# Kernel optimization log

Measured on AMD Instinct MI355X. Metric: run time of the kernel, lower is better.

Reference implementation:

```python
import jax, jax.numpy as jnp
import numpy as np

NUM_QRYS = 300
NUM_CLASSES = 80
NUM_PAIRS = 4_000_000
NMS_CANDIDATES = 1000
NMS_THR = 0.65
MAX_SEGS = 100
REFINED_WEIGHT = 2.0
FH = FW = 256  # final mask grid resolution


def setup_inputs() -> dict:
    key = jax.random.key(0)
    k1, k2, k3, k4, k5, k6, k7 = jax.random.split(key, 7)
    cls_logits = jax.random.normal(k1, (NUM_QRYS, NUM_CLASSES + 1), jnp.float32)
    # valid xyxy boxes in normalized [0,1] coords
    b = jax.random.uniform(k2, (NUM_QRYS, 4), jnp.float32)
    x1 = b[:, 0] * 0.7
    y1 = b[:, 1] * 0.7
    x2 = x1 + 0.05 + b[:, 2] * 0.25
    y2 = y1 + 0.05 + b[:, 3] * 0.25
    pred_boxes = jnp.stack([x1, y1, x2, y2], axis=1)
    seg_logits = jax.random.normal(k3, (NUM_PAIRS,), jnp.float32)
    key_xy = jax.random.uniform(k4, (NUM_PAIRS, 2), jnp.float32)
    qry_ids = jax.random.randint(k5, (NUM_PAIRS,), 0, NUM_QRYS, jnp.int32)
    refined_mask = jax.random.randint(k6, (NUM_PAIRS,), 0, 2, jnp.int32).astype(bool)
    map_ids = jax.random.randint(k7, (NUM_PAIRS,), 0, 4, jnp.int32)
    return {"cls_logits": cls_logits, "pred_boxes": pred_boxes, "seg_logits": seg_logits,
            "key_xy": key_xy, "qry_ids": qry_ids, "refined_mask": refined_mask, "map_ids": map_ids}


def _box_iou(boxes):  # boxes: [C,4] xyxy -> [C,C]
    x1 = jnp.maximum(boxes[:, None, 0], boxes[None, :, 0])
    y1 = jnp.maximum(boxes[:, None, 1], boxes[None, :, 1])
    x2 = jnp.minimum(boxes[:, None, 2], boxes[None, :, 2])
    y2 = jnp.minimum(boxes[:, None, 3], boxes[None, :, 3])
    inter = jnp.clip(x2 - x1, 0.0) * jnp.clip(y2 - y1, 0.0)
    area = (boxes[:, 2] - boxes[:, 0]) * (boxes[:, 3] - boxes[:, 1])
    union = area[:, None] + area[None, :] - inter
    return inter / jnp.maximum(union, 1e-9)


def _nms_keep(iou, thr):
    # greedy NMS over score-sorted candidates (rows already in descending score order)
    C = iou.shape[0]
    idx = jnp.arange(C)
    def body(i, keep):
        sup = (iou[i] > thr) & (idx > i) & keep[i]
        return keep & ~sup
    return jax.lax.fori_loop(0, C, body, jnp.ones(C, dtype=bool))


def reference(cls_logits, pred_boxes, seg_logits, key_xy, qry_ids, refined_mask, map_ids):
    num_qrys = cls_logits.shape[0]
    # expand per-query class scores -> flat predictions (batch_size = 1)
    scores = jax.nn.sigmoid(cls_logits[:, :-1]).reshape(-1)          # [Q*C]
    feat_ids = jnp.repeat(jnp.arange(num_qrys), NUM_CLASSES)          # [Q*C]
    labels = jnp.tile(jnp.arange(NUM_CLASSES), num_qrys)              # [Q*C]
    # top-k candidates before NMS
    top_scores, cand = jax.lax.top_k(scores, NMS_CANDIDATES)
    cand_feats = feat_ids[cand]
    cand_labels = labels[cand]
    # class-aware (batched) NMS: offset boxes per label so classes don't suppress each other
    offs = cand_labels.astype(pred_boxes.dtype)[:, None] * 4.0
    cand_boxes = pred_boxes[cand_feats] + offs
    keep = _nms_keep(_box_iou(cand_boxes), NMS_THR)
    kept_scores = jnp.where(keep, top_scores, -jnp.inf)
    sel_scores, sel = jax.lax.top_k(kept_scores, MAX_SEGS)
    sel_scores = jnp.where(jnp.isfinite(sel_scores), sel_scores, 0.0)
    sel_feats = cand_feats[sel]
    # assemble per-query mask logit maps from sparse query-key pairs (scatter-max)
    px = jnp.clip((key_xy[:, 0] * FW).astype(jnp.int32), 0, FW - 1)
    py = jnp.clip((key_xy[:, 1] * FH).astype(jnp.int32), 0, FH - 1)
    w_logits = jnp.where(refined_mask, REFINED_WEIGHT * seg_logits, seg_logits)
    flat = qry_ids * (FH * FW) + py * FW + px                          # [num_pairs]
    qry_maps = jnp.full((num_qrys * FH * FW,), -1e4, cls_logits.dtype).at[flat].max(w_logits)
    qry_maps = qry_maps.reshape(num_qrys, FH, FW)
    mask_probs = jax.nn.sigmoid(qry_maps[sel_feats])                   # [MAX_SEGS, FH, FW]
    # score-weighted soft masks (float output; thresholding at mask_thr yields bool masks)
    return sel_scores[:, None, None] * mask_probs
```

## Files before the change

### kernel.cpp

```cpp
#include <hip/hip_runtime.h>

#define NQ        300
#define NC        80
#define NE        24000
#define CAND      1000
#define KSEL      100
#define NPAIRS    4000000
#define HB        4096
#define FHW       65536
#define NMS_THR_F 0.65f
#define MAPS_INIT 0x39E3BFFFu
#define INIT_VEC4 1638400

typedef unsigned long long ull;

__device__ __forceinline__ unsigned enc_f32(float f) {
    unsigned u = __float_as_uint(f);
    return (u & 0x80000000u) ? ~u : (u | 0x80000000u);
}
__device__ __forceinline__ float dec_f32(unsigned k) {
    unsigned u = (k & 0x80000000u) ? (k ^ 0x80000000u) : ~k;
    return __uint_as_float(u);
}

__global__ __launch_bounds__(1024) void k_front(
    const float* __restrict__ cls,
    const float* __restrict__ pboxes,
    const unsigned* __restrict__ refined_raw,
    uint4* __restrict__ maps4, ull* __restrict__ keys_g,
    float* __restrict__ sel_score_g, int* __restrict__ sel_slot_g,
    int* __restrict__ qry2slot_g, unsigned* __restrict__ mode_flag_g)
{
    if (blockIdx.x > 0) {
        uint4 v; v.x = v.y = v.z = v.w = MAPS_INIT;
        for (int i = (int)(blockIdx.x - 1) * 1024 + (int)threadIdx.x;
             i < INIT_VEC4; i += 256 * 1024)
            maps4[i] = v;
        return;
    }

    __shared__ ull sbuf[4096];
    __shared__ float sbx[CAND], sby[CAND], sbz[CAND], sbw[CAND];
    __shared__ float sscore[CAND];
    __shared__ short sfeat[CAND];
    __shared__ unsigned char slab[CAND];
    __shared__ unsigned char skeep[CAND];
    __shared__ int wlist[16][64];
    __shared__ int q2s[NQ];
    __shared__ float ss[KSEL]; __shared__ int sf[KSEL];
    __shared__ unsigned subhist[64];
    __shared__ unsigned smode;
    __shared__ int sB, sT, sAbove, sCount, sN;

    unsigned* hist = (unsigned*)sbuf;
    int tid = threadIdx.x;
    int lane = tid & 63, wv = tid >> 6;

    for (int b = tid; b < HB; b += 1024) hist[b] = 0u;
    if (tid < 64) subhist[tid] = 0u;
    if (tid == 0) { smode = 0u; sCount = 0; sB = 0; sAbove = 0; }
    __syncthreads();

    #pragma unroll
    for (int k = 0; k < 24; k++) {
        int e = tid + (k << 10);
        if (e < NE) {
            int q = e / NC, c = e - q * NC;
            float x = cls[q * (NC + 1) + c];
            float s = 1.f / (1.f + expf(-x));
            unsigned bits = __float_as_uint(s);
            keys_g[e] = ((ull)bits << 32) | (unsigned)(0xFFFFFFFFu - (unsigned)e);
            atomicAdd(&hist[bits >> 18], 1u);
        }
    }
    if (refined_raw[tid] > 1u) atomicOr(&smode, 1u);
    __syncthreads();

    if (tid < 64) {
        int acc = 0;
        for (int base = HB - 64; base >= 0; base -= 64) {
            unsigned h = hist[base + lane];
            unsigned r = h;
            #pragma unroll
            for (int d = 1; d < 64; d <<= 1) {
                unsigned t2 = __shfl_down(r, d, 64);
                if (lane + d < 64) r += t2;
            }
            ull m = __ballot(acc + (int)r >= CAND);
            if (m) {
                int hi = 63 - __clzll(m);
                int rB = __shfl((int)r, hi, 64);
                int hB = __shfl((int)h, hi, 64);
                if (lane == 0) { sB = base + hi; sAbove = acc + rB - hB; }
                break;
            }
            acc += __shfl((int)r, 0, 64);
        }
    }
    __syncthreads();
    unsigned B = (unsigned)sB;

    #pragma unroll
    for (int k = 0; k < 24; k++) {
        int e = tid + (k << 10);
        if (e < NE) {
            ull key = keys_g[e];
            if ((unsigned)(key >> 50) == B)
                atomicAdd(&subhist[(unsigned)(key >> 44) & 63u], 1u);
        }
    }
    __syncthreads();
    if (tid < 64) {
        unsigned h = subhist[lane];
        unsigned r = h;
        #pragma unroll
        for (int d = 1; d < 64; d <<= 1) {
            unsigned t2 = __shfl_down(r, d, 64);
            if (lane + d < 64) r += t2;
        }
        int above = sAbove;
        ull m = __ballot(above + (int)r >= CAND);
        int hi = 63 - __clzll(m);
        int rT = __shfl((int)r, hi, 64);
        if (lane == 0) { sT = hi; sN = above + rT; }
    }
    __syncthreads();
    unsigned T = (unsigned)sT;

    #pragma unroll
    for (int k = 0; k < 24; k++) {
        int e = tid + (k << 10);
        if (e < NE) {
            ull key = keys_g[e];
            unsigned bkt = (unsigned)(key >> 50);
            unsigned sub = (unsigned)(key >> 44) & 63u;
            if (bkt > B || (bkt == B && sub >= T)) {
                int pos = atomicAdd(&sCount, 1);
                if (pos < 4096) sbuf[pos] = key;
            }
        }
    }
    __syncthreads();
    int n = min(sN, 4096);

    if (n <= 1024) {
        ull r = (tid < n) ? sbuf[tid] : 0ULL;
        for (int k = 2; k <= 1024; k <<= 1) {
            for (int j = k >> 1; j > 0; j >>= 1) {
                ull p;
                if (j >= 64) {
                    sbuf[tid] = r; __syncthreads();
                    p = sbuf[tid ^ j]; __syncthreads();
                } else {
                    p = __shfl_xor(r, j, 64);
                }
                bool d = (tid & k) != 0, lower = (tid & j) == 0;
                r = (d != lower) ? (r > p ? r : p) : (r < p ? r : p);
            }
        }
        sbuf[tid] = r;
        __syncthreads();
    } else {
        int nsort = 2048; while (nsort < n) nsort <<= 1;
        for (int i = n + tid; i < nsort; i += 1024) sbuf[i] = 0ULL;
        __syncthreads();
        for (int k = 2; k <= nsort; k <<= 1)
            for (int j = k >> 1; j > 0; j >>= 1) {
                for (int i = tid; i < nsort; i += 1024) {
                    int ixj = i ^ j;
                    if (ixj > i) {
                        ull a = sbuf[i], b2 = sbuf[ixj];
                        bool up = ((i & k) == 0);
                        if (up ? (a < b2) : (a > b2)) { sbuf[i] = b2; sbuf[ixj] = a; }
                    }
                }
                __syncthreads();
            }
    }

    if (tid < CAND) {
        ull key = sbuf[tid];
        unsigned bits = (unsigned)(key >> 32);
        unsigned e = 0xFFFFFFFFu - (unsigned)(key & 0xFFFFFFFFu);
        int feat = (int)e / NC, lab = (int)e - feat * NC;
        sscore[tid] = __uint_as_float(bits);
        sfeat[tid]  = (short)feat;
        slab[tid]   = (unsigned char)lab;
        float off = 4.f * (float)lab;
        const float4 pb = ((const float4*)pboxes)[feat];
        sbx[tid] = pb.x + off; sby[tid] = pb.y + off;
        sbz[tid] = pb.z + off; sbw[tid] = pb.w + off;
    }
    __syncthreads();

    for (int li = 0; li < 5; li++) {
        int lab = wv + (li << 4);
        int nb = 0;
        for (int c = 0; c < CAND; c += 64) {
            int i = c + lane;
            bool m = (i < CAND) && ((int)slab[i] == lab);
            ull bal = __ballot(m);
            if (m) {
                int r = nb + __popcll(bal & ((1ULL << lane) - 1ULL));
                if (r < 64) wlist[wv][r] = i;
            }
            nb += __popcll(bal);
        }
        int nl = min(nb, 64);
        __syncthreads();

        bool alive = lane < nl;
        float bxv = 0.f, byv = 0.f, bzv = 0.f, bwv = 0.f, ar = 0.f;
        int idx = -1;
        if (alive) {
            idx = wlist[wv][lane];
            bxv = sbx[idx]; byv = sby[idx]; bzv = sbz[idx]; bwv = sbw[idx];
            ar = (bzv - bxv) * (bwv - byv);
        }
        bool keep = alive;
        for (int i = 0; i < nl; i++) {
            float bix = __shfl(bxv, i), biy = __shfl(byv, i);
            float biz = __shfl(bzv, i), biw = __shfl(bwv, i);
            float ai  = __shfl(ar, i);
            int   ki  = __shfl((int)keep, i);
            if (ki && keep && lane > i) {
                float xx1 = fmaxf(bix, bxv), yy1 = fmaxf(biy, byv);
                float xx2 = fminf(biz, bzv), yy2 = fminf(biw, bwv);
                float inter = fmaxf(xx2 - xx1, 0.f) * fmaxf(yy2 - yy1, 0.f);
                float uni = ai + ar - inter;
                if (inter / fmaxf(uni, 1e-9f) > NMS_THR_F) keep = false;
            }
        }
        if (alive) skeep[idx] = keep ? 1 : 0;
    }
    __syncthreads();

    for (int q = tid; q < NQ; q += 1024) q2s[q] = -1;
    __syncthreads();
    if (tid < 64) {
        int base = 0;
        for (int c = 0; c < CAND; c += 64) {
            int i = c + lane;
            bool k2 = (i < CAND) && skeep[i];
            ull bal = __ballot(k2);
            int pos = base + __popcll(bal & ((1ULL << lane) - 1ULL));
            if (k2 && pos < KSEL) { ss[pos] = sscore[i]; sf[pos] = (int)sfeat[i]; }
            base += __popcll(bal);
        }
        int nsel = min(base, KSEL);
        int s1 = lane, s2 = lane + 64;
        int fp1 = s1, fp2 = s2;
        if (s1 < nsel) { int f = sf[s1]; for (int k2 = 0; k2 < s1; k2++) if (sf[k2] == f) { fp1 = k2; break; } }
        if (s2 < nsel) { int f = sf[s2]; for (int k2 = 0; k2 < s2; k2++) if (sf[k2] == f) { fp2 = k2; break; } }
        bool fo1 = (s1 < nsel) && (fp1 == s1);
        bool fo2 = (s2 < nsel) && (fp2 == s2);
        ull b1 = __ballot(fo1);
        ull b2 = __ballot(fo2);
        int c1 = __popcll(b1);
        int slot1 = -1, slot2 = -1;
        if (s1 < nsel) slot1 = __popcll(b1 & ((1ULL << fp1) - 1ULL));
        if (s2 < nsel) slot2 = (fp2 < 64) ? __popcll(b1 & ((1ULL << fp2) - 1ULL))
                                          : c1 + __popcll(b2 & ((1ULL << (fp2 - 64)) - 1ULL));
        sel_slot_g[s1] = slot1;
        sel_score_g[s1] = (s1 < nsel) ? ss[s1] : 0.f;
        if (s2 < KSEL) {
            sel_slot_g[s2] = slot2;
            sel_score_g[s2] = (s2 < nsel) ? ss[s2] : 0.f;
        }
        if (fo1) q2s[sf[s1]] = slot1;
        if (fo2) q2s[sf[s2]] = slot2;
        if (lane == 0) *mode_flag_g = smode;
    }
    __syncthreads();
    for (int q = tid; q < NQ; q += 1024) qry2slot_g[q] = q2s[q];
}

__global__ __launch_bounds__(256) void k_scatter(
    const float* __restrict__ seg, const float2* __restrict__ xy,
    const int* __restrict__ qry, const unsigned* __restrict__ refined_raw,
    const int* __restrict__ qry2slot, const unsigned* __restrict__ mode_flag,
    unsigned* __restrict__ maps)
{
    int t = blockIdx.x * 256 + threadIdx.x;
    if ((t << 2) >= NPAIRS) return;

    int4 q4     = ((const int4*)qry)[t];
    float4 sg   = ((const float4*)seg)[t];
    float4 xy01 = ((const float4*)xy)[2 * t];
    float4 xy23 = ((const float4*)xy)[2 * t + 1];
    unsigned r0, r1, r2, r3;
    if (*mode_flag) {
        unsigned rb = refined_raw[t];
        r0 = rb & 255u; r1 = (rb >> 8) & 255u; r2 = (rb >> 16) & 255u; r3 = rb >> 24;
    } else {
        uint4 rr = ((const uint4*)refined_raw)[t];
        r0 = rr.x; r1 = rr.y; r2 = rr.z; r3 = rr.w;
    }
    int s0 = qry2slot[q4.x], s1 = qry2slot[q4.y];
    int s2 = qry2slot[q4.z], s3 = qry2slot[q4.w];

    #define DO_PAIR(S, PX, PY, W, R)                                              \
        if (S >= 0) {                                                             \
            int px = min(max((int)((PX) * 256.f), 0), 255);                       \
            int py = min(max((int)((PY) * 256.f), 0), 255);                       \
            float w = (R) ? 2.f * (W) : (W);                                      \
            atomicMax(&maps[S * FHW + py * 256 + px], enc_f32(w));                \
        }
    DO_PAIR(s0, xy01.x, xy01.y, sg.x, r0)
    DO_PAIR(s1, xy01.z, xy01.w, sg.y, r1)
    DO_PAIR(s2, xy23.x, xy23.y, sg.z, r2)
    DO_PAIR(s3, xy23.z, xy23.w, sg.w, r3)
    #undef DO_PAIR
}

__global__ __launch_bounds__(256) void k_output(
    const uint4* __restrict__ maps4,
    const float* __restrict__ sel_score, const int* __restrict__ sel_slot,
    float4* __restrict__ out4)
{
    int i = blockIdx.x * 256 + threadIdx.x;
    int s = i >> 14;
    float sc = sel_score[s];
    int slot = sel_slot[s];
    float4 v = {0.f, 0.f, 0.f, 0.f};
    if (slot >= 0) {
        uint4 m = maps4[slot * (FHW / 4) + (i & 16383)];
        v.x = sc / (1.f + expf(-dec_f32(m.x)));
        v.y = sc / (1.f + expf(-dec_f32(m.y)));
        v.z = sc / (1.f + expf(-dec_f32(m.z)));
        v.w = sc / (1.f + expf(-dec_f32(m.w)));
    }
    out4[i] = v;
}

extern "C" void kernel_launch(void* const* d_in, const int* in_sizes, int n_in,
                              void* d_out, int out_size, void* d_ws, size_t ws_size,
                              hipStream_t stream) {
    const float*    cls     = (const float*)d_in[0];
    const float*    pboxes  = (const float*)d_in[1];
    const float*    seg     = (const float*)d_in[2];
    const float2*   xy      = (const float2*)d_in[3];
    const int*      qry     = (const int*)d_in[4];
    const unsigned* refined = (const unsigned*)d_in[5];
    float* out = (float*)d_out;

    char* ws = (char*)d_ws;
    unsigned*  maps      = (unsigned*)ws;
    float*     sel_score = (float*)   (ws + 26214400);
    int*       sel_slot  = (int*)     (ws + 26214800);
    int*       qry2slot  = (int*)     (ws + 26215200);
    unsigned*  mode_flag = (unsigned*)(ws + 26216400);
    ull*       keys      = (ull*)d_out;

    k_front  <<<257, 1024, 0, stream>>>(cls, pboxes, refined, (uint4*)maps, keys,
                                        sel_score, sel_slot, qry2slot, mode_flag);
    k_scatter<<<3907, 256, 0, stream>>>(seg, xy, qry, refined, qry2slot, mode_flag, maps);
    k_output <<<6400, 256, 0, stream>>>((const uint4*)maps, sel_score, sel_slot,
                                        (float4*)out);
}
```

Before: 253.4 us.

## Split monolithic front kernel into multi-block init, histogram, boundary, sort and NMS stages

Breaks the single-block front kernel into separate launches. Map init and the sigmoid/key/histogram work now run across many blocks, and a finer 65536-bin global histogram locates the top-1000 boundary in one pass, with no sub-histogram refinement. The serial single-block part now covers only the 2048-wide bitonic sort and the NMS. The cost is more kernel launches and global-memory handoffs between the stages. The sort buffer is capped at 2048, which assumes boundary-bucket ties stay small.

```diff
diff --git a/kernel.cpp b/kernel.cpp
--- a/kernel.cpp
+++ b/kernel.cpp
@@ -6,11 +6,10 @@
 #define CAND      1000
 #define KSEL      100
 #define NPAIRS    4000000
-#define HB        4096
+#define HBN       65536
 #define FHW       65536
 #define NMS_THR_F 0.65f
 #define MAPS_INIT 0x39E3BFFFu
-#define INIT_VEC4 1638400
 
 typedef unsigned long long ull;
 
@@ -23,125 +22,93 @@
     return __uint_as_float(u);
 }
 
-__global__ __launch_bounds__(1024) void k_front(
-    const float* __restrict__ cls,
-    const float* __restrict__ pboxes,
-    const unsigned* __restrict__ refined_raw,
-    uint4* __restrict__ maps4, ull* __restrict__ keys_g,
-    float* __restrict__ sel_score_g, int* __restrict__ sel_slot_g,
-    int* __restrict__ qry2slot_g, unsigned* __restrict__ mode_flag_g)
-{
-    if (blockIdx.x > 0) {
+__global__ void k_init(uint4* __restrict__ maps4, unsigned* __restrict__ hist,
+                       unsigned* __restrict__ mode_flag) {
+    int b = blockIdx.x, tid = threadIdx.x;
+    if (b < 6400) {
         uint4 v; v.x = v.y = v.z = v.w = MAPS_INIT;
-        for (int i = (int)(blockIdx.x - 1) * 1024 + (int)threadIdx.x;
-             i < INIT_VEC4; i += 256 * 1024)
-            maps4[i] = v;
-        return;
-    }
-
-    __shared__ ull sbuf[4096];
-    __shared__ float sbx[CAND], sby[CAND], sbz[CAND], sbw[CAND];
-    __shared__ float sscore[CAND];
-    __shared__ short sfeat[CAND];
-    __shared__ unsigned char slab[CAND];
-    __shared__ unsigned char skeep[CAND];
-    __shared__ int wlist[16][64];
-    __shared__ int q2s[NQ];
-    __shared__ float ss[KSEL]; __shared__ int sf[KSEL];
-    __shared__ unsigned subhist[64];
-    __shared__ unsigned smode;
-    __shared__ int sB, sT, sAbove, sCount, sN;
-
-    unsigned* hist = (unsigned*)sbuf;
+        maps4[b * 256 + tid] = v;
+    } else {
+        int j = (b - 6400) * 256 + tid;
+        if (j < HBN) hist[j] = 0u;
+        if (j == HBN) *mode_flag = 0u;
+    }
+}
+
+__global__ __launch_bounds__(256) void k_sigkeys(
+    const float* __restrict__ cls, const unsigned* __restrict__ refined_raw,
+    ull* __restrict__ keys_g, unsigned* __restrict__ hist,
+    unsigned* __restrict__ mode_flag)
+{
     int tid = threadIdx.x;
-    int lane = tid & 63, wv = tid >> 6;
-
-    for (int b = tid; b < HB; b += 1024) hist[b] = 0u;
-    if (tid < 64) subhist[tid] = 0u;
-    if (tid == 0) { smode = 0u; sCount = 0; sB = 0; sAbove = 0; }
-    __syncthreads();
-
-    #pragma unroll
-    for (int k = 0; k < 24; k++) {
-        int e = tid + (k << 10);
-        if (e < NE) {
-            int q = e / NC, c = e - q * NC;
-            float x = cls[q * (NC + 1) + c];
-            float s = 1.f / (1.f + expf(-x));
-            unsigned bits = __float_as_uint(s);
-            keys_g[e] = ((ull)bits << 32) | (unsigned)(0xFFFFFFFFu - (unsigned)e);
-            atomicAdd(&hist[bits >> 18], 1u);
-        }
-    }
-    if (refined_raw[tid] > 1u) atomicOr(&smode, 1u);
-    __syncthreads();
-
-    if (tid < 64) {
-        int acc = 0;
-        for (int base = HB - 64; base >= 0; base -= 64) {
-            unsigned h = hist[base + lane];
-            unsigned r = h;
-            #pragma unroll
-            for (int d = 1; d < 64; d <<= 1) {
-                unsigned t2 = __shfl_down(r, d, 64);
-                if (lane + d < 64) r += t2;
-            }
-            ull m = __ballot(acc + (int)r >= CAND);
-            if (m) {
-                int hi = 63 - __clzll(m);
-                int rB = __shfl((int)r, hi, 64);
-                int hB = __shfl((int)h, hi, 64);
-                if (lane == 0) { sB = base + hi; sAbove = acc + rB - hB; }
-                break;
-            }
-            acc += __shfl((int)r, 0, 64);
-        }
-    }
-    __syncthreads();
-    unsigned B = (unsigned)sB;
+    int e = blockIdx.x * 256 + tid;
+    if (e < NE) {
+        int q = e / NC, c = e - q * NC;
+        float x = cls[q * (NC + 1) + c];
+        float s = 1.f / (1.f + expf(-x));
+        unsigned bits = __float_as_uint(s);
+        keys_g[e] = ((ull)bits << 32) | (unsigned)(0xFFFFFFFFu - (unsigned)e);
+        atomicAdd(&hist[min(bits >> 14, (unsigned)(HBN - 1))], 1u);
+    }
+    if (blockIdx.x == 0) {
+        unsigned bad = 0;
+        #pragma unroll
+        for (int j = 0; j < 4; j++) bad |= (refined_raw[tid + 256 * j] > 1u) ? 1u : 0u;
+        if (bad) atomicOr(mode_flag, 1u);
+    }
+}
+
+__global__ __launch_bounds__(64) void k_boundary(
+    const unsigned* __restrict__ hist, int* __restrict__ bn)
+{
+    int lane = threadIdx.x;
+    int acc = 0;
+    for (int base = HBN - 64; base >= 0; base -= 64) {
+        unsigned h = hist[base + lane];
+        unsigned r = h;
+        #pragma unroll
+        for (int d = 1; d < 64; d <<= 1) {
+            unsigned t2 = __shfl_down(r, d, 64);
+            if (lane + d < 64) r += t2;
+        }
+        ull m = __ballot(acc + (int)r >= CAND);
+        if (m) {
+            int hi = 63 - __clzll(m);
+            int rB = __shfl((int)r, hi, 64);
+            if (lane == 0) { bn[0] = base + hi; bn[1] = acc + rB; }
+            return;
+        }
+        acc += __shfl((int)r, 0, 64);
+    }
+    if (lane == 0) { bn[0] = 0; bn[1] = NE; }
+}
+
+__global__ __launch_bounds__(1024) void k_sortsel(
+    const ull* __restrict__ keys_g, const float* __restrict__ pboxes,
+    const int* __restrict__ bn,
+    float4* __restrict__ cboxes, float* __restrict__ cscore,
+    int* __restrict__ cfeat, int* __restrict__ clabel)
+{
+    __shared__ ull sbuf[2048];
+    __shared__ int sCount;
+    int tid = threadIdx.x;
+    if (tid == 0) sCount = 0;
+    __syncthreads();
+    unsigned B = (unsigned)bn[0];
 
     #pragma unroll
     for (int k = 0; k < 24; k++) {
         int e = tid + (k << 10);
         if (e < NE) {
             ull key = keys_g[e];
-            if ((unsigned)(key >> 50) == B)
-                atomicAdd(&subhist[(unsigned)(key >> 44) & 63u], 1u);
-        }
-    }
-    __syncthreads();
-    if (tid < 64) {
-        unsigned h = subhist[lane];
-        unsigned r = h;
-        #pragma unroll
-        for (int d = 1; d < 64; d <<= 1) {
-            unsigned t2 = __shfl_down(r, d, 64);
-            if (lane + d < 64) r += t2;
-        }
-        int above = sAbove;
-        ull m = __ballot(above + (int)r >= CAND);
-        int hi = 63 - __clzll(m);
-        int rT = __shfl((int)r, hi, 64);
-        if (lane == 0) { sT = hi; sN = above + rT; }
-    }
-    __syncthreads();
-    unsigned T = (unsigned)sT;
-
-    #pragma unroll
-    for (int k = 0; k < 24; k++) {
-        int e = tid + (k << 10);
-        if (e < NE) {
-            ull key = keys_g[e];
-            unsigned bkt = (unsigned)(key >> 50);
-            unsigned sub = (unsigned)(key >> 44) & 63u;
-            if (bkt > B || (bkt == B && sub >= T)) {
+            if ((unsigned)(key >> 46) >= B) {
                 int pos = atomicAdd(&sCount, 1);
-                if (pos < 4096) sbuf[pos] = key;
-            }
-        }
-    }
-    __syncthreads();
-    int n = min(sN, 4096);
+                if (pos < 2048) sbuf[pos] = key;
+            }
+        }
+    }
+    __syncthreads();
+    int n = min(sCount, 2048);
 
     if (n <= 1024) {
         ull r = (tid < n) ? sbuf[tid] : 0ULL;
@@ -161,12 +128,11 @@
         sbuf[tid] = r;
         __syncthreads();
     } else {
-        int nsort = 2048; while (nsort < n) nsort <<= 1;
-        for (int i = n + tid; i < nsort; i += 1024) sbuf[i] = 0ULL;
+        for (int i = n + tid; i < 2048; i += 1024) sbuf[i] = 0ULL;
         __syncthreads();
-        for (int k = 2; k <= nsort; k <<= 1)
+        for (int k = 2; k <= 2048; k <<= 1)
             for (int j = k >> 1; j > 0; j >>= 1) {
-                for (int i = tid; i < nsort; i += 1024) {
+                for (int i = tid; i < 2048; i += 1024) {
                     int ixj = i ^ j;
                     if (ixj > i) {
                         ull a = sbuf[i], b2 = sbuf[ixj];
@@ -183,22 +149,35 @@
         unsigned bits = (unsigned)(key >> 32);
         unsigned e = 0xFFFFFFFFu - (unsigned)(key & 0xFFFFFFFFu);
         int feat = (int)e / NC, lab = (int)e - feat * NC;
-        sscore[tid] = __uint_as_float(bits);
-        sfeat[tid]  = (short)feat;
-        slab[tid]   = (unsigned char)lab;
+        cscore[tid] = __uint_as_float(bits);
+        cfeat[tid]  = feat;
+        clabel[tid] = lab;
         float off = 4.f * (float)lab;
-        const float4 pb = ((const float4*)pboxes)[feat];
-        sbx[tid] = pb.x + off; sby[tid] = pb.y + off;
-        sbz[tid] = pb.z + off; sbw[tid] = pb.w + off;
-    }
-    __syncthreads();
+        float4 pb = ((const float4*)pboxes)[feat];
+        float4 b;
+        b.x = pb.x + off; b.y = pb.y + off; b.z = pb.z + off; b.w = pb.w + off;
+        cboxes[tid] = b;
+    }
+}
+
+__global__ __launch_bounds__(1024) void k_nms_pick(
+    const float4* __restrict__ cboxes, const float* __restrict__ cscore,
+    const int* __restrict__ cfeat, const int* __restrict__ clabel,
+    float* __restrict__ sel_score_g, int* __restrict__ sel_slot_g,
+    int* __restrict__ qry2slot_g)
+{
+    __shared__ unsigned char skeep[CAND];
+    __shared__ int wlist[16][64];
+    __shared__ int q2s[NQ];
+    __shared__ float ss[KSEL]; __shared__ int sf[KSEL];
+    int tid = threadIdx.x, lane = tid & 63, wv = tid >> 6;
 
     for (int li = 0; li < 5; li++) {
         int lab = wv + (li << 4);
         int nb = 0;
         for (int c = 0; c < CAND; c += 64) {
             int i = c + lane;
-            bool m = (i < CAND) && ((int)slab[i] == lab);
+            bool m = (i < CAND) && (clabel[i] == lab);
             ull bal = __ballot(m);
             if (m) {
                 int r = nb + __popcll(bal & ((1ULL << lane) - 1ULL));
@@ -214,7 +193,8 @@
         int idx = -1;
         if (alive) {
             idx = wlist[wv][lane];
-            bxv = sbx[idx]; byv = sby[idx]; bzv = sbz[idx]; bwv = sbw[idx];
+            float4 cb = cboxes[idx];
+            bxv = cb.x; byv = cb.y; bzv = cb.z; bwv = cb.w;
             ar = (bzv - bxv) * (bwv - byv);
         }
         bool keep = alive;
@@ -244,7 +224,7 @@
             bool k2 = (i < CAND) && skeep[i];
             ull bal = __ballot(k2);
             int pos = base + __popcll(bal & ((1ULL << lane) - 1ULL));
-            if (k2 && pos < KSEL) { ss[pos] = sscore[i]; sf[pos] = (int)sfeat[i]; }
+            if (k2 && pos < KSEL) { ss[pos] = cscore[i]; sf[pos] = cfeat[i]; }
             base += __popcll(bal);
         }
         int nsel = min(base, KSEL);
@@ -269,7 +249,6 @@
         }
         if (fo1) q2s[sf[s1]] = slot1;
         if (fo2) q2s[sf[s2]] = slot2;
-        if (lane == 0) *mode_flag_g = smode;
     }
     __syncthreads();
     for (int q = tid; q < NQ; q += 1024) qry2slot_g[q] = q2s[q];
@@ -344,17 +323,29 @@
     const unsigned* refined = (const unsigned*)d_in[5];
     float* out = (float*)d_out;
 
+    char* ob = (char*)d_out;
+    ull*      keys   = (ull*)ob;
+    unsigned* hist   = (unsigned*)(ob + 196608);
+    float4*   cboxes = (float4*)(ob + 458752);
+    float*    cscore = (float*)(ob + 474752);
+    int*      cfeat  = (int*)(ob + 478752);
+    int*      clabel = (int*)(ob + 482752);
+    int*      bn     = (int*)(ob + 486752);
+
     char* ws = (char*)d_ws;
-    unsigned*  maps      = (unsigned*)ws;
-    float*     sel_score = (float*)   (ws + 26214400);
-    int*       sel_slot  = (int*)     (ws + 26214800);
-    int*       qry2slot  = (int*)     (ws + 26215200);
-    unsigned*  mode_flag = (unsigned*)(ws + 26216400);
-    ull*       keys      = (ull*)d_out;
-
-    k_front  <<<257, 1024, 0, stream>>>(cls, pboxes, refined, (uint4*)maps, keys,
-                                        sel_score, sel_slot, qry2slot, mode_flag);
-    k_scatter<<<3907, 256, 0, stream>>>(seg, xy, qry, refined, qry2slot, mode_flag, maps);
-    k_output <<<6400, 256, 0, stream>>>((const uint4*)maps, sel_score, sel_slot,
-                                        (float4*)out);
-}
+    unsigned* maps      = (unsigned*)ws;
+    float*    sel_score = (float*)   (ws + 26214400);
+    int*      sel_slot  = (int*)     (ws + 26214800);
+    int*      qry2slot  = (int*)     (ws + 26215200);
+    unsigned* mode_flag = (unsigned*)(ws + 26216400);
+
+    k_init    <<<6657, 256, 0, stream>>>((uint4*)maps, hist, mode_flag);
+    k_sigkeys <<<94, 256, 0, stream>>>(cls, refined, keys, hist, mode_flag);
+    k_boundary<<<1, 64, 0, stream>>>(hist, bn);
+    k_sortsel <<<1, 1024, 0, stream>>>(keys, pboxes, bn, cboxes, cscore, cfeat, clabel);
+    k_nms_pick<<<1, 1024, 0, stream>>>(cboxes, cscore, cfeat, clabel,
+                                       sel_score, sel_slot, qry2slot);
+    k_scatter <<<3907, 256, 0, stream>>>(seg, xy, qry, refined, qry2slot, mode_flag, maps);
+    k_output  <<<6400, 256, 0, stream>>>((const uint4*)maps, sel_score, sel_slot,
+                                         (float4*)out);
+}
```

Result: no change. 254.4 us (+0.4%).

## Fuse all stages into one cooperative persistent kernel with grid syncs

Applied to the files above, without the earlier changes.

Merges the front (top-k, NMS), scatter and output kernels into a single cooperative kernel of 256 blocks of 1024 threads, separated by grid.sync barriers. The candidate histogram is built grid-wide with a finer 65536-bucket global histogram, replacing the two-level shared-memory selection. This removes launch gaps between kernels, but the scatter and output stages now run at the lower occupancy of a persistent grid, and several grid syncs are added. The single-block sort and NMS phase still serialises while the other blocks wait at the barrier.

```diff
diff --git a/kernel.cpp b/kernel.cpp
--- a/kernel.cpp
+++ b/kernel.cpp
@@ -1,4 +1,7 @@
 #include <hip/hip_runtime.h>
+#include <hip/hip_cooperative_groups.h>
+
+namespace cg = cooperative_groups;
 
 #define NQ        300
 #define NC        80
@@ -6,11 +9,13 @@
 #define CAND      1000
 #define KSEL      100
 #define NPAIRS    4000000
-#define HB        4096
+#define HBN       65536
 #define FHW       65536
 #define NMS_THR_F 0.65f
 #define MAPS_INIT 0x39E3BFFFu
-#define INIT_VEC4 1638400
+#define GBLK      256
+#define GTH       262144
+#define MAPS_V4   1638400
 
 typedef unsigned long long ull;
 
@@ -23,314 +28,283 @@
     return __uint_as_float(u);
 }
 
-__global__ __launch_bounds__(1024) void k_front(
+__global__ __launch_bounds__(1024) void k_mega(
     const float* __restrict__ cls,
     const float* __restrict__ pboxes,
-    const unsigned* __restrict__ refined_raw,
-    uint4* __restrict__ maps4, ull* __restrict__ keys_g,
-    float* __restrict__ sel_score_g, int* __restrict__ sel_slot_g,
-    int* __restrict__ qry2slot_g, unsigned* __restrict__ mode_flag_g)
+    const float* __restrict__ seg, const float2* __restrict__ xy,
+    const int* __restrict__ qry, const unsigned* __restrict__ refined,
+    unsigned* __restrict__ maps, ull* __restrict__ keys,
+    unsigned* __restrict__ hist, ull* __restrict__ cand,
+    int* __restrict__ cand_count,
+    float* __restrict__ sel_score, int* __restrict__ sel_slot,
+    int* __restrict__ qry2slot, unsigned* __restrict__ mode_flag,
+    float* __restrict__ out)
 {
-    if (blockIdx.x > 0) {
-        uint4 v; v.x = v.y = v.z = v.w = MAPS_INIT;
-        for (int i = (int)(blockIdx.x - 1) * 1024 + (int)threadIdx.x;
-             i < INIT_VEC4; i += 256 * 1024)
-            maps4[i] = v;
-        return;
-    }
-
-    __shared__ ull sbuf[4096];
+    cg::grid_group grid = cg::this_grid();
+    const int tid = threadIdx.x, bid = blockIdx.x;
+    const int flat = bid * 1024 + tid;
+    const int lane = tid & 63;
+
+    __shared__ ull sbuf[2048];
     __shared__ float sbx[CAND], sby[CAND], sbz[CAND], sbw[CAND];
     __shared__ float sscore[CAND];
     __shared__ short sfeat[CAND];
-    __shared__ unsigned char slab[CAND];
-    __shared__ unsigned char skeep[CAND];
+    __shared__ unsigned char slab[CAND], skeep[CAND];
     __shared__ int wlist[16][64];
     __shared__ int q2s[NQ];
     __shared__ float ss[KSEL]; __shared__ int sf[KSEL];
-    __shared__ unsigned subhist[64];
-    __shared__ unsigned smode;
-    __shared__ int sB, sT, sAbove, sCount, sN;
-
-    unsigned* hist = (unsigned*)sbuf;
-    int tid = threadIdx.x;
-    int lane = tid & 63, wv = tid >> 6;
-
-    for (int b = tid; b < HB; b += 1024) hist[b] = 0u;
-    if (tid < 64) subhist[tid] = 0u;
-    if (tid == 0) { smode = 0u; sCount = 0; sB = 0; sAbove = 0; }
-    __syncthreads();
-
-    #pragma unroll
-    for (int k = 0; k < 24; k++) {
-        int e = tid + (k << 10);
-        if (e < NE) {
-            int q = e / NC, c = e - q * NC;
-            float x = cls[q * (NC + 1) + c];
-            float s = 1.f / (1.f + expf(-x));
-            unsigned bits = __float_as_uint(s);
-            keys_g[e] = ((ull)bits << 32) | (unsigned)(0xFFFFFFFFu - (unsigned)e);
-            atomicAdd(&hist[bits >> 18], 1u);
-        }
-    }
-    if (refined_raw[tid] > 1u) atomicOr(&smode, 1u);
-    __syncthreads();
-
-    if (tid < 64) {
-        int acc = 0;
-        for (int base = HB - 64; base >= 0; base -= 64) {
-            unsigned h = hist[base + lane];
-            unsigned r = h;
-            #pragma unroll
-            for (int d = 1; d < 64; d <<= 1) {
-                unsigned t2 = __shfl_down(r, d, 64);
-                if (lane + d < 64) r += t2;
-            }
-            ull m = __ballot(acc + (int)r >= CAND);
-            if (m) {
-                int hi = 63 - __clzll(m);
-                int rB = __shfl((int)r, hi, 64);
-                int hB = __shfl((int)h, hi, 64);
-                if (lane == 0) { sB = base + hi; sAbove = acc + rB - hB; }
-                break;
-            }
-            acc += __shfl((int)r, 0, 64);
-        }
-    }
-    __syncthreads();
-    unsigned B = (unsigned)sB;
-
-    #pragma unroll
-    for (int k = 0; k < 24; k++) {
-        int e = tid + (k << 10);
-        if (e < NE) {
-            ull key = keys_g[e];
-            if ((unsigned)(key >> 50) == B)
-                atomicAdd(&subhist[(unsigned)(key >> 44) & 63u], 1u);
-        }
-    }
-    __syncthreads();
-    if (tid < 64) {
-        unsigned h = subhist[lane];
-        unsigned r = h;
-        #pragma unroll
-        for (int d = 1; d < 64; d <<= 1) {
-            unsigned t2 = __shfl_down(r, d, 64);
-            if (lane + d < 64) r += t2;
-        }
-        int above = sAbove;
-        ull m = __ballot(above + (int)r >= CAND);
-        int hi = 63 - __clzll(m);
-        int rT = __shfl((int)r, hi, 64);
-        if (lane == 0) { sT = hi; sN = above + rT; }
-    }
-    __syncthreads();
-    unsigned T = (unsigned)sT;
-
-    #pragma unroll
-    for (int k = 0; k < 24; k++) {
-        int e = tid + (k << 10);
-        if (e < NE) {
-            ull key = keys_g[e];
-            unsigned bkt = (unsigned)(key >> 50);
-            unsigned sub = (unsigned)(key >> 44) & 63u;
-            if (bkt > B || (bkt == B && sub >= T)) {
-                int pos = atomicAdd(&sCount, 1);
-                if (pos < 4096) sbuf[pos] = key;
-            }
-        }
-    }
-    __syncthreads();
-    int n = min(sN, 4096);
-
-    if (n <= 1024) {
-        ull r = (tid < n) ? sbuf[tid] : 0ULL;
-        for (int k = 2; k <= 1024; k <<= 1) {
-            for (int j = k >> 1; j > 0; j >>= 1) {
-                ull p;
-                if (j >= 64) {
-                    sbuf[tid] = r; __syncthreads();
-                    p = sbuf[tid ^ j]; __syncthreads();
-                } else {
-                    p = __shfl_xor(r, j, 64);
-                }
-                bool d = (tid & k) != 0, lower = (tid & j) == 0;
-                r = (d != lower) ? (r > p ? r : p) : (r < p ? r : p);
-            }
-        }
-        sbuf[tid] = r;
-        __syncthreads();
-    } else {
-        int nsort = 2048; while (nsort < n) nsort <<= 1;
-        for (int i = n + tid; i < nsort; i += 1024) sbuf[i] = 0ULL;
-        __syncthreads();
-        for (int k = 2; k <= nsort; k <<= 1)
-            for (int j = k >> 1; j > 0; j >>= 1) {
-                for (int i = tid; i < nsort; i += 1024) {
-                    int ixj = i ^ j;
-                    if (ixj > i) {
-                        ull a = sbuf[i], b2 = sbuf[ixj];
-                        bool up = ((i & k) == 0);
-                        if (up ? (a < b2) : (a > b2)) { sbuf[i] = b2; sbuf[ixj] = a; }
+    __shared__ int sB;
+    __shared__ unsigned smode_l;
+
+    {
+        uint4 v; v.x = v.y = v.z = v.w = MAPS_INIT;
+        uint4* maps4 = (uint4*)maps;
+        for (int i = flat; i < MAPS_V4; i += GTH) maps4[i] = v;
+        if (flat < HBN) hist[flat] = 0u;
+        if (flat == 0) *cand_count = 0;
+    }
+    grid.sync();
+
+    if (flat < NE) {
+        int q = flat / NC, c = flat - q * NC;
+        float x = cls[q * (NC + 1) + c];
+        float s = 1.f / (1.f + expf(-x));
+        unsigned bits = __float_as_uint(s);
+        keys[flat] = ((ull)bits << 32) | (unsigned)(0xFFFFFFFFu - (unsigned)flat);
+        atomicAdd(&hist[min(bits >> 14, (unsigned)(HBN - 1))], 1u);
+    }
+    if (bid == 24) {
+        if (tid == 0) smode_l = 0u;
+        __syncthreads();
+        if (refined[tid] > 1u) atomicOr(&smode_l, 1u);
+        __syncthreads();
+        if (tid == 0) *mode_flag = smode_l;
+    }
+    grid.sync();
+
+    if (bid < 24) {
+        if (tid < 64) {
+            int acc = 0;
+            for (int b2 = HBN - 64; b2 >= 0; b2 -= 64) {
+                unsigned h = hist[b2 + lane];
+                unsigned r = h;
+                #pragma unroll
+                for (int d = 1; d < 64; d <<= 1) {
+                    unsigned t2 = __shfl_down(r, d, 64);
+                    if (lane + d < 64) r += t2;
+                }
+                ull m = __ballot(acc + (int)r >= CAND);
+                if (m) {
+                    if (lane == 0) sB = b2 + (63 - __clzll(m));
+                    break;
+                }
+                acc += __shfl((int)r, 0, 64);
+            }
+        }
+        __syncthreads();
+        unsigned B = (unsigned)sB;
+        bool q = false; ull key = 0ULL;
+        if (flat < NE) {
+            key = keys[flat];
+            q = ((unsigned)(key >> 46) >= B);
+        }
+        ull bal = __ballot(q);
+        int rank = __popcll(bal & ((1ULL << lane) - 1ULL));
+        int base = 0;
+        if (lane == 0 && bal) base = atomicAdd(cand_count, (int)__popcll(bal));
+        base = __shfl(base, 0, 64);
+        if (q) cand[base + rank] = key;
+    }
+    grid.sync();
+
+    if (bid == 0) {
+        int n = min(*cand_count, 2048);
+        for (int i = tid; i < 2048; i += 1024) sbuf[i] = (i < n) ? cand[i] : 0ULL;
+        __syncthreads();
+
+        if (n <= 1024) {
+            ull r = sbuf[tid];
+            for (int k = 2; k <= 1024; k <<= 1) {
+                for (int j = k >> 1; j > 0; j >>= 1) {
+                    ull p;
+                    if (j >= 64) {
+                        sbuf[tid] = r; __syncthreads();
+                        p = sbuf[tid ^ j]; __syncthreads();
+                    } else {
+                        p = __shfl_xor(r, j, 64);
                     }
-                }
-                __syncthreads();
-            }
-    }
-
-    if (tid < CAND) {
-        ull key = sbuf[tid];
-        unsigned bits = (unsigned)(key >> 32);
-        unsigned e = 0xFFFFFFFFu - (unsigned)(key & 0xFFFFFFFFu);
-        int feat = (int)e / NC, lab = (int)e - feat * NC;
-        sscore[tid] = __uint_as_float(bits);
-        sfeat[tid]  = (short)feat;
-        slab[tid]   = (unsigned char)lab;
-        float off = 4.f * (float)lab;
-        const float4 pb = ((const float4*)pboxes)[feat];
-        sbx[tid] = pb.x + off; sby[tid] = pb.y + off;
-        sbz[tid] = pb.z + off; sbw[tid] = pb.w + off;
-    }
-    __syncthreads();
-
-    for (int li = 0; li < 5; li++) {
-        int lab = wv + (li << 4);
-        int nb = 0;
-        for (int c = 0; c < CAND; c += 64) {
-            int i = c + lane;
-            bool m = (i < CAND) && ((int)slab[i] == lab);
-            ull bal = __ballot(m);
-            if (m) {
-                int r = nb + __popcll(bal & ((1ULL << lane) - 1ULL));
-                if (r < 64) wlist[wv][r] = i;
-            }
-            nb += __popcll(bal);
-        }
-        int nl = min(nb, 64);
-        __syncthreads();
-
-        bool alive = lane < nl;
-        float bxv = 0.f, byv = 0.f, bzv = 0.f, bwv = 0.f, ar = 0.f;
-        int idx = -1;
-        if (alive) {
-            idx = wlist[wv][lane];
-            bxv = sbx[idx]; byv = sby[idx]; bzv = sbz[idx]; bwv = sbw[idx];
-            ar = (bzv - bxv) * (bwv - byv);
-        }
-        bool keep = alive;
-        for (int i = 0; i < nl; i++) {
-            float bix = __shfl(bxv, i), biy = __shfl(byv, i);
-            float biz = __shfl(bzv, i), biw = __shfl(bwv, i);
-            float ai  = __shfl(ar, i);
-            int   ki  = __shfl((int)keep, i);
-            if (ki && keep && lane > i) {
-                float xx1 = fmaxf(bix, bxv), yy1 = fmaxf(biy, byv);
-                float xx2 = fminf(biz, bzv), yy2 = fminf(biw, bwv);
-                float inter = fmaxf(xx2 - xx1, 0.f) * fmaxf(yy2 - yy1, 0.f);
-                float uni = ai + ar - inter;
-                if (inter / fmaxf(uni, 1e-9f) > NMS_THR_F) keep = false;
-            }
-        }
-        if (alive) skeep[idx] = keep ? 1 : 0;
-    }
-    __syncthreads();
-
-    for (int q = tid; q < NQ; q += 1024) q2s[q] = -1;
-    __syncthreads();
-    if (tid < 64) {
-        int base = 0;
-        for (int c = 0; c < CAND; c += 64) {
-            int i = c + lane;
-            bool k2 = (i < CAND) && skeep[i];
-            ull bal = __ballot(k2);
-            int pos = base + __popcll(bal & ((1ULL << lane) - 1ULL));
-            if (k2 && pos < KSEL) { ss[pos] = sscore[i]; sf[pos] = (int)sfeat[i]; }
-            base += __popcll(bal);
-        }
-        int nsel = min(base, KSEL);
-        int s1 = lane, s2 = lane + 64;
-        int fp1 = s1, fp2 = s2;
-        if (s1 < nsel) { int f = sf[s1]; for (int k2 = 0; k2 < s1; k2++) if (sf[k2] == f) { fp1 = k2; break; } }
-        if (s2 < nsel) { int f = sf[s2]; for (int k2 = 0; k2 < s2; k2++) if (sf[k2] == f) { fp2 = k2; break; } }
-        bool fo1 = (s1 < nsel) && (fp1 == s1);
-        bool fo2 = (s2 < nsel) && (fp2 == s2);
-        ull b1 = __ballot(fo1);
-        ull b2 = __ballot(fo2);
-        int c1 = __popcll(b1);
-        int slot1 = -1, slot2 = -1;
-        if (s1 < nsel) slot1 = __popcll(b1 & ((1ULL << fp1) - 1ULL));
-        if (s2 < nsel) slot2 = (fp2 < 64) ? __popcll(b1 & ((1ULL << fp2) - 1ULL))
-                                          : c1 + __popcll(b2 & ((1ULL << (fp2 - 64)) - 1ULL));
-        sel_slot_g[s1] = slot1;
-        sel_score_g[s1] = (s1 < nsel) ? ss[s1] : 0.f;
-        if (s2 < KSEL) {
-            sel_slot_g[s2] = slot2;
-            sel_score_g[s2] = (s2 < nsel) ? ss[s2] : 0.f;
-        }
-        if (fo1) q2s[sf[s1]] = slot1;
-        if (fo2) q2s[sf[s2]] = slot2;
-        if (lane == 0) *mode_flag_g = smode;
-    }
-    __syncthreads();
-    for (int q = tid; q < NQ; q += 1024) qry2slot_g[q] = q2s[q];
-}
-
-__global__ __launch_bounds__(256) void k_scatter(
-    const float* __restrict__ seg, const float2* __restrict__ xy,
-    const int* __restrict__ qry, const unsigned* __restrict__ refined_raw,
-    const int* __restrict__ qry2slot, const unsigned* __restrict__ mode_flag,
-    unsigned* __restrict__ maps)
-{
-    int t = blockIdx.x * 256 + threadIdx.x;
-    if ((t << 2) >= NPAIRS) return;
-
-    int4 q4     = ((const int4*)qry)[t];
-    float4 sg   = ((const float4*)seg)[t];
-    float4 xy01 = ((const float4*)xy)[2 * t];
-    float4 xy23 = ((const float4*)xy)[2 * t + 1];
-    unsigned r0, r1, r2, r3;
-    if (*mode_flag) {
-        unsigned rb = refined_raw[t];
-        r0 = rb & 255u; r1 = (rb >> 8) & 255u; r2 = (rb >> 16) & 255u; r3 = rb >> 24;
-    } else {
-        uint4 rr = ((const uint4*)refined_raw)[t];
-        r0 = rr.x; r1 = rr.y; r2 = rr.z; r3 = rr.w;
-    }
-    int s0 = qry2slot[q4.x], s1 = qry2slot[q4.y];
-    int s2 = qry2slot[q4.z], s3 = qry2slot[q4.w];
-
-    #define DO_PAIR(S, PX, PY, W, R)                                              \
-        if (S >= 0) {                                                             \
-            int px = min(max((int)((PX) * 256.f), 0), 255);                       \
-            int py = min(max((int)((PY) * 256.f), 0), 255);                       \
-            float w = (R) ? 2.f * (W) : (W);                                      \
-            atomicMax(&maps[S * FHW + py * 256 + px], enc_f32(w));                \
-        }
-    DO_PAIR(s0, xy01.x, xy01.y, sg.x, r0)
-    DO_PAIR(s1, xy01.z, xy01.w, sg.y, r1)
-    DO_PAIR(s2, xy23.x, xy23.y, sg.z, r2)
-    DO_PAIR(s3, xy23.z, xy23.w, sg.w, r3)
-    #undef DO_PAIR
-}
-
-__global__ __launch_bounds__(256) void k_output(
-    const uint4* __restrict__ maps4,
-    const float* __restrict__ sel_score, const int* __restrict__ sel_slot,
-    float4* __restrict__ out4)
-{
-    int i = blockIdx.x * 256 + threadIdx.x;
-    int s = i >> 14;
-    float sc = sel_score[s];
-    int slot = sel_slot[s];
-    float4 v = {0.f, 0.f, 0.f, 0.f};
-    if (slot >= 0) {
-        uint4 m = maps4[slot * (FHW / 4) + (i & 16383)];
-        v.x = sc / (1.f + expf(-dec_f32(m.x)));
-        v.y = sc / (1.f + expf(-dec_f32(m.y)));
-        v.z = sc / (1.f + expf(-dec_f32(m.z)));
-        v.w = sc / (1.f + expf(-dec_f32(m.w)));
-    }
-    out4[i] = v;
+                    bool d = (tid & k) != 0, lower = (tid & j) == 0;
+                    r = (d != lower) ? (r > p ? r : p) : (r < p ? r : p);
+                }
+            }
+            sbuf[tid] = r;
+            __syncthreads();
+        } else {
+            for (int k = 2; k <= 2048; k <<= 1)
+                for (int j = k >> 1; j > 0; j >>= 1) {
+                    for (int i = tid; i < 2048; i += 1024) {
+                        int ixj = i ^ j;
+                        if (ixj > i) {
+                            ull a = sbuf[i], b2 = sbuf[ixj];
+                            bool up = ((i & k) == 0);
+                            if (up ? (a < b2) : (a > b2)) { sbuf[i] = b2; sbuf[ixj] = a; }
+                        }
+                    }
+                    __syncthreads();
+                }
+        }
+
+        if (tid < CAND) {
+            ull key = sbuf[tid];
+            unsigned bits = (unsigned)(key >> 32);
+            unsigned e = 0xFFFFFFFFu - (unsigned)(key & 0xFFFFFFFFu);
+            int feat = (int)e / NC, lab = (int)e - feat * NC;
+            sscore[tid] = __uint_as_float(bits);
+            sfeat[tid]  = (short)feat;
+            slab[tid]   = (unsigned char)lab;
+            skeep[tid]  = 0;
+            float off = 4.f * (float)lab;
+            float4 pb = ((const float4*)pboxes)[feat];
+            sbx[tid] = pb.x + off; sby[tid] = pb.y + off;
+            sbz[tid] = pb.z + off; sbw[tid] = pb.w + off;
+        }
+        __syncthreads();
+
+        int wv = tid >> 6;
+        for (int li = 0; li < 5; li++) {
+            int lab = wv + (li << 4);
+            int nb = 0;
+            for (int c = 0; c < CAND; c += 64) {
+                int i = c + lane;
+                bool m = (i < CAND) && ((int)slab[i] == lab);
+                ull bal = __ballot(m);
+                if (m) {
+                    int r = nb + __popcll(bal & ((1ULL << lane) - 1ULL));
+                    if (r < 64) wlist[wv][r] = i;
+                }
+                nb += __popcll(bal);
+            }
+            int nl = min(nb, 64);
+            __syncthreads();
+
+            bool alive = lane < nl;
+            float bxv = 0.f, byv = 0.f, bzv = 0.f, bwv = 0.f, ar = 0.f;
+            int idx = -1;
+            if (alive) {
+                idx = wlist[wv][lane];
+                bxv = sbx[idx]; byv = sby[idx]; bzv = sbz[idx]; bwv = sbw[idx];
+                ar = (bzv - bxv) * (bwv - byv);
+            }
+            bool keep = alive;
+            for (int i = 0; i < nl; i++) {
+                float bix = __shfl(bxv, i), biy = __shfl(byv, i);
+                float biz = __shfl(bzv, i), biw = __shfl(bwv, i);
+                float ai  = __shfl(ar, i);
+                int   ki  = __shfl((int)keep, i);
+                if (ki && keep && lane > i) {
+                    float xx1 = fmaxf(bix, bxv), yy1 = fmaxf(biy, byv);
+                    float xx2 = fminf(biz, bzv), yy2 = fminf(biw, bwv);
+                    float inter = fmaxf(xx2 - xx1, 0.f) * fmaxf(yy2 - yy1, 0.f);
+                    float uni = ai + ar - inter;
+                    if (inter / fmaxf(uni, 1e-9f) > NMS_THR_F) keep = false;
+                }
+            }
+            if (alive) skeep[idx] = keep ? 1 : 0;
+        }
+        __syncthreads();
+
+        for (int q = tid; q < NQ; q += 1024) q2s[q] = -1;
+        __syncthreads();
+        if (tid < 64) {
+            int base = 0;
+            for (int c = 0; c < CAND; c += 64) {
+                int i = c + lane;
+                bool k2 = (i < CAND) && skeep[i];
+                ull bal = __ballot(k2);
+                int pos = base + __popcll(bal & ((1ULL << lane) - 1ULL));
+                if (k2 && pos < KSEL) { ss[pos] = sscore[i]; sf[pos] = (int)sfeat[i]; }
+                base += __popcll(bal);
+            }
+            int nsel = min(base, KSEL);
+            int s1 = lane, s2 = lane + 64;
+            int fp1 = s1, fp2 = s2;
+            if (s1 < nsel) { int f = sf[s1]; for (int k2 = 0; k2 < s1; k2++) if (sf[k2] == f) { fp1 = k2; break; } }
+            if (s2 < nsel) { int f = sf[s2]; for (int k2 = 0; k2 < s2; k2++) if (sf[k2] == f) { fp2 = k2; break; } }
+            bool fo1 = (s1 < nsel) && (fp1 == s1);
+            bool fo2 = (s2 < nsel) && (fp2 == s2);
+            ull b1 = __ballot(fo1);
+            ull b2 = __ballot(fo2);
+            int c1 = __popcll(b1);
+            int slot1 = -1, slot2 = -1;
+            if (s1 < nsel) slot1 = __popcll(b1 & ((1ULL << fp1) - 1ULL));
+            if (s2 < nsel) slot2 = (fp2 < 64) ? __popcll(b1 & ((1ULL << fp2) - 1ULL))
+                                              : c1 + __popcll(b2 & ((1ULL << (fp2 - 64)) - 1ULL));
+            sel_slot[s1] = slot1;
+            sel_score[s1] = (s1 < nsel) ? ss[s1] : 0.f;
+            if (s2 < KSEL) {
+                sel_slot[s2] = slot2;
+                sel_score[s2] = (s2 < nsel) ? ss[s2] : 0.f;
+            }
+            if (fo1) q2s[sf[s1]] = slot1;
+            if (fo2) q2s[sf[s2]] = slot2;
+        }
+        __syncthreads();
+        for (int q = tid; q < NQ; q += 1024) qry2slot[q] = q2s[q];
+    }
+    grid.sync();
+
+    {
+        unsigned mode = *mode_flag;
+        for (int g = flat; g < NPAIRS / 4; g += GTH) {
+            int4 q4     = ((const int4*)qry)[g];
+            float4 sg   = ((const float4*)seg)[g];
+            float4 xy01 = ((const float4*)xy)[2 * g];
+            float4 xy23 = ((const float4*)xy)[2 * g + 1];
+            unsigned r0, r1, r2, r3;
+            if (mode) {
+                unsigned rb = refined[g];
+                r0 = rb & 255u; r1 = (rb >> 8) & 255u; r2 = (rb >> 16) & 255u; r3 = rb >> 24;
+            } else {
+                uint4 rr = ((const uint4*)refined)[g];
+                r0 = rr.x; r1 = rr.y; r2 = rr.z; r3 = rr.w;
+            }
+            int s0 = qry2slot[q4.x], s1 = qry2slot[q4.y];
+            int s2 = qry2slot[q4.z], s3 = qry2slot[q4.w];
+
+            #define DO_PAIR(S, PX, PY, W, R)                                      \
+                if (S >= 0) {                                                     \
+                    int px = min(max((int)((PX) * 256.f), 0), 255);               \
+                    int py = min(max((int)((PY) * 256.f), 0), 255);               \
+                    float w = (R) ? 2.f * (W) : (W);                              \
+                    atomicMax(&maps[S * FHW + py * 256 + px], enc_f32(w));        \
+                }
+            DO_PAIR(s0, xy01.x, xy01.y, sg.x, r0)
+            DO_PAIR(s1, xy01.z, xy01.w, sg.y, r1)
+            DO_PAIR(s2, xy23.x, xy23.y, sg.z, r2)
+            DO_PAIR(s3, xy23.z, xy23.w, sg.w, r3)
+            #undef DO_PAIR
+        }
+    }
+    grid.sync();
+
+    {
+        const uint4* maps4 = (const uint4*)maps;
+        float4* out4 = (float4*)out;
+        for (int i = flat; i < MAPS_V4; i += GTH) {
+            int s = i >> 14;
+            float sc = sel_score[s];
+            int slot = sel_slot[s];
+            float4 v = {0.f, 0.f, 0.f, 0.f};
+            if (slot >= 0) {
+                uint4 m = maps4[slot * (FHW / 4) + (i & 16383)];
+                v.x = sc / (1.f + expf(-dec_f32(m.x)));
+                v.y = sc / (1.f + expf(-dec_f32(m.y)));
+                v.z = sc / (1.f + expf(-dec_f32(m.z)));
+                v.w = sc / (1.f + expf(-dec_f32(m.w)));
+            }
+            out4[i] = v;
+        }
+    }
 }
 
 extern "C" void kernel_launch(void* const* d_in, const int* in_sizes, int n_in,
@@ -344,17 +318,24 @@
     const unsigned* refined = (const unsigned*)d_in[5];
     float* out = (float*)d_out;
 
+    char* ob = (char*)d_out;
+    ull*      keys  = (ull*)ob;
+    unsigned* hist  = (unsigned*)(ob + 196608);
+    ull*      cand  = (ull*)(ob + 458752);
+
     char* ws = (char*)d_ws;
-    unsigned*  maps      = (unsigned*)ws;
-    float*     sel_score = (float*)   (ws + 26214400);
-    int*       sel_slot  = (int*)     (ws + 26214800);
-    int*       qry2slot  = (int*)     (ws + 26215200);
-    unsigned*  mode_flag = (unsigned*)(ws + 26216400);
-    ull*       keys      = (ull*)d_out;
-
-    k_front  <<<257, 1024, 0, stream>>>(cls, pboxes, refined, (uint4*)maps, keys,
-                                        sel_score, sel_slot, qry2slot, mode_flag);
-    k_scatter<<<3907, 256, 0, stream>>>(seg, xy, qry, refined, qry2slot, mode_flag, maps);
-    k_output <<<6400, 256, 0, stream>>>((const uint4*)maps, sel_score, sel_slot,
-                                        (float4*)out);
+    unsigned* maps       = (unsigned*)ws;
+    float*    sel_score  = (float*)   (ws + 26214400);
+    int*      sel_slot   = (int*)     (ws + 26214800);
+    int*      qry2slot   = (int*)     (ws + 26215200);
+    unsigned* mode_flag  = (unsigned*)(ws + 26216400);
+    int*      cand_count = (int*)     (ws + 26216404);
+
+    void* args[] = {
+        (void*)&cls, (void*)&pboxes, (void*)&seg, (void*)&xy, (void*)&qry,
+        (void*)&refined, (void*)&maps, (void*)&keys, (void*)&hist, (void*)&cand,
+        (void*)&cand_count, (void*)&sel_score, (void*)&sel_slot, (void*)&qry2slot,
+        (void*)&mode_flag, (void*)&out
+    };
+    hipLaunchCooperativeKernel((void*)k_mega, dim3(GBLK), dim3(1024), args, 0, stream);
 }
```

Measured after the change: 378.4 us. +49.3%, slower.
